# Kernel tuning notes

Hardware: AMD Instinct MI355X
Metric: run time of the kernel (lower is better)

The kernel has to match this reference:

```python
import jax, jax.numpy as jnp
import numpy as np

N, IN, OUT = 8192, 4096, 16384


def setup_inputs() -> dict:
    key = jax.random.key(0)
    kx, kw, kb = jax.random.split(key, 3)
    x = jax.random.normal(kx, (N, IN), dtype=jnp.float32)
    # init matches reset_parameters: normal(0, sqrt(1/in_features))
    weight = jax.random.normal(kw, (OUT, IN), dtype=jnp.float32) * np.sqrt(1.0 / IN)
    bias = jax.random.normal(kb, (OUT,), dtype=jnp.float32) * 0.02
    return {"x": x, "weight": weight, "bias": bias}


def _ternarize(weight):
    # threshold = 0.5 * mean(|W|); zero out |w| < threshold, else sign(w)
    threshold = 0.5 * jnp.mean(jnp.abs(weight))
    keep = jnp.abs(weight) >= threshold
    ternary_weight = jnp.sign(weight) * keep.astype(weight.dtype)
    return ternary_weight


def reference(x, weight, bias):
    tw = _ternarize(weight)              # [out, in] in {-1, 0, 1}
    out = x @ tw.T + bias                # [N, out]
    return out
```

## Files before the change

kernel.cpp:

```cpp
#include <hip/hip_runtime.h>
#include <hip/hip_bf16.h>
#include <cstdint>
#include <cstddef>

#define M_DIM 8192
#define K_DIM 4096
#define N_DIM 16384

#define BM 256
#define BN 256
#define BK 32
#define NT (K_DIM / BK)
#define GX (N_DIM / BN)
#define GY (M_DIM / BM)

typedef __attribute__((ext_vector_type(8))) short short8;
typedef __attribute__((ext_vector_type(4))) float floatx4;

__device__ inline void gl2lds16(const void* g, void* l) {
  __builtin_amdgcn_global_load_lds(
      (const __attribute__((address_space(1))) void*)g,
      (__attribute__((address_space(3))) void*)l, 16, 0, 0);
}

__global__ void abssum_kernel(const float* __restrict__ w, double* __restrict__ out) {
  size_t tid = (size_t)blockIdx.x * blockDim.x + threadIdx.x;
  size_t stride = (size_t)gridDim.x * blockDim.x;
  const float4* w4 = (const float4*)w;
  const size_t n4 = (size_t)N_DIM * K_DIM / 4;
  double s = 0.0;
  for (size_t i = tid; i < n4; i += stride) {
    float4 v = w4[i];
    s += (double)fabsf(v.x) + (double)fabsf(v.y) + (double)fabsf(v.z) + (double)fabsf(v.w);
  }
  #pragma unroll
  for (int off = 32; off > 0; off >>= 1) s += __shfl_down(s, off, 64);
  if ((threadIdx.x & 63) == 0) atomicAdd(out, s);
}

__global__ void ternarize_kernel(const float* __restrict__ w, ushort* __restrict__ tw,
                                 const double* __restrict__ sum) {
  __shared__ float sthr;
  if (threadIdx.x == 0)
    sthr = (float)(0.5 * (*sum) / (double)((size_t)N_DIM * K_DIM));
  __syncthreads();
  const float thr = sthr;
  size_t i = ((size_t)blockIdx.x * blockDim.x + threadIdx.x) * 8;
  float4 a = *(const float4*)(w + i);
  float4 b = *(const float4*)(w + i + 4);
  float v[8] = {a.x, a.y, a.z, a.w, b.x, b.y, b.z, b.w};
  union { ushort u[8]; uint4 q; } o;
  #pragma unroll
  for (int j = 0; j < 8; j++) {
    float av = fabsf(v[j]);
    o.u[j] = (av >= thr) ? ((v[j] > 0.0f) ? (ushort)0x3F80 : (ushort)0xBF80) : (ushort)0;
  }
  *(uint4*)(tw + i) = o.q;
}

__device__ inline ushort f2bf(float f) {
  uint32_t u = __float_as_uint(f);
  return (ushort)((u + 0x7FFFu + ((u >> 16) & 1u)) >> 16);
}
__global__ void bf16cast_kernel(const float* __restrict__ x, ushort* __restrict__ xb) {
  size_t i = ((size_t)blockIdx.x * blockDim.x + threadIdx.x) * 8;
  float4 a = *(const float4*)(x + i);
  float4 b = *(const float4*)(x + i + 4);
  float v[8] = {a.x, a.y, a.z, a.w, b.x, b.y, b.z, b.w};
  union { ushort u[8]; uint4 q; } o;
  #pragma unroll
  for (int j = 0; j < 8; j++) o.u[j] = f2bf(v[j]);
  *(uint4*)(xb + i) = o.q;
}

__global__ __launch_bounds__(512, 2)
void gemm_bt_kernel(const ushort* __restrict__ A, const ushort* __restrict__ B,
                    const float* __restrict__ bias, float* __restrict__ C) {
  __shared__ __align__(128) ushort As[4][BM * BK];
  __shared__ __align__(128) ushort Bs[4][BN * BK];

  const int tid  = threadIdx.x;
  const int wave = tid >> 6;
  const int lane = tid & 63;
  const int wm   = wave >> 2;
  const int wn   = wave & 3;
  const int r16  = lane & 15;
  const int quad = lane >> 4;

  const int f  = (int)(blockIdx.y * GX + blockIdx.x);
  const int xc = f & 7;
  const int j  = f >> 3;
  const int p  = j >> 5;
  const int k  = j & 31;
  const int pm = p >> 2, pn = p & 3;
  const int bm = pm * 16 + ((xc >> 2) << 3) + (k & 7);
  const int bn = pn * 16 + ((xc & 3) << 2) + (k >> 3);

  const int bsw = ((lane >> 2) ^ (lane >> 4)) & 1;
  const int rr  = ((lane >> 3) << 1) | bsw;
  const int qb1 = ((lane >> 1) ^ (lane >> 3)) & 1;
  const int qb0 = (lane ^ (lane >> 2) ^ (lane >> 4)) & 1;
  const int qq  = (qb1 << 1) | qb0;
  const int srow = wave * 16 + rr;
  const int scol = qq * 8;
  const ushort* pA0 = A + (size_t)(bm * BM + srow) * K_DIM + scol;
  const ushort* pA1 = pA0 + (size_t)128 * K_DIM;
  const ushort* pB0 = B + (size_t)(bn * BN + srow) * K_DIM + scol;
  const ushort* pB1 = pB0 + (size_t)128 * K_DIM;
  const int ldsw = wave * 16 * BK;

#define STAGE_A(T) do { const int _b = (T) & 3;                        \
    gl2lds16(pA0 + (size_t)(T) * BK, &As[_b][ldsw]);                   \
    gl2lds16(pA1 + (size_t)(T) * BK, &As[_b][128 * BK + ldsw]); } while (0)
#define STAGE_B(T) do { const int _b = (T) & 3;                        \
    gl2lds16(pB0 + (size_t)(T) * BK, &Bs[_b][ldsw]);                   \
    gl2lds16(pB1 + (size_t)(T) * BK, &Bs[_b][128 * BK + ldsw]); } while (0)

  floatx4 acc[8][4];
  #pragma unroll
  for (int m = 0; m < 8; m++)
    #pragma unroll
    for (int n = 0; n < 4; n++)
      acc[m][n] = (floatx4){0.f, 0.f, 0.f, 0.f};

  STAGE_A(0); STAGE_B(0);
  STAGE_A(1); STAGE_B(1);
  STAGE_A(2); STAGE_B(2);
  STAGE_A(3);
  asm volatile("s_waitcnt vmcnt(10)" ::: "memory");
  __builtin_amdgcn_s_barrier();

  const int inner = ((r16 << 6) + (quad << 4)) ^ ((r16 & 7) << 4);
  const char* aBytes; const char* bBytes;

  for (int t = 0; t < NT; ++t) {
    const int cb = t & 3;
    aBytes = (const char*)(&As[cb][0]) + wm * 8192 + inner;
    bBytes = (const char*)(&Bs[cb][0]) + wn * 4096 + inner;
    short8 a[8], b[4];
    #pragma unroll
    for (int m = 0; m < 4; ++m) a[m] = *(const short8*)(aBytes + m * 1024);
    #pragma unroll
    for (int n = 0; n < 4; ++n) b[n] = *(const short8*)(bBytes + n * 1024);
    __builtin_amdgcn_sched_barrier(0);
    #pragma unroll
    for (int m = 4; m < 8; ++m) a[m] = *(const short8*)(aBytes + m * 1024);
    if (t + 3 < NT) STAGE_B(t + 3);
    __builtin_amdgcn_sched_barrier(0);
    __builtin_amdgcn_s_barrier();
    asm volatile("s_waitcnt lgkmcnt(4)" ::: "memory");
    __builtin_amdgcn_sched_barrier(0);
    __builtin_amdgcn_s_setprio(1);
    #pragma unroll
    for (int m = 0; m < 4; ++m)
      #pragma unroll
      for (int n = 0; n < 4; ++n)
        acc[m][n] = __builtin_amdgcn_mfma_f32_16x16x32_bf16(a[m], b[n], acc[m][n], 0, 0, 0);
    __builtin_amdgcn_s_setprio(0);
    __builtin_amdgcn_s_barrier();
    if (t + 4 < NT) {
      STAGE_A(t + 4);
      asm volatile("s_waitcnt vmcnt(10)" ::: "memory");
    } else {
      asm volatile("s_waitcnt vmcnt(0)" ::: "memory");
    }
    __builtin_amdgcn_s_barrier();
    asm volatile("s_waitcnt lgkmcnt(0)" ::: "memory");
    __builtin_amdgcn_sched_barrier(0);
    __builtin_amdgcn_s_setprio(1);
    #pragma unroll
    for (int m = 4; m < 8; ++m)
      #pragma unroll
      for (int n = 0; n < 4; ++n)
        acc[m][n] = __builtin_amdgcn_mfma_f32_16x16x32_bf16(a[m], b[n], acc[m][n], 0, 0, 0);
    __builtin_amdgcn_s_setprio(0);
    __builtin_amdgcn_s_barrier();
  }

  const int crow = bm * BM + wm * 128 + quad * 4;
  const int ccol = bn * BN + wn * 64 + r16;
  #pragma unroll
  for (int n = 0; n < 4; ++n) {
    const int col = ccol + n * 16;
    const float bv = bias[col];
    #pragma unroll
    for (int m = 0; m < 8; ++m) {
      const size_t row0 = (size_t)(crow + m * 16);
      #pragma unroll
      for (int r = 0; r < 4; ++r)
        __builtin_nontemporal_store(acc[m][n][r] + bv, &C[(row0 + r) * N_DIM + col]);
    }
  }
#undef STAGE_A
#undef STAGE_B
}

extern "C" void kernel_launch(void* const* d_in, const int* in_sizes, int n_in,
                              void* d_out, int out_size, void* d_ws, size_t ws_size,
                              hipStream_t stream) {
  const float* x    = (const float*)d_in[0];
  const float* w    = (const float*)d_in[1];
  const float* bias = (const float*)d_in[2];
  float* out = (float*)d_out;

  char* ws = (char*)d_ws;
  double* sum = (double*)ws;
  ushort* xb  = (ushort*)(ws + 256);
  ushort* tw  = (ushort*)(ws + 256 + (size_t)M_DIM * K_DIM * 2);

  hipMemsetAsync(sum, 0, sizeof(double), stream);
  abssum_kernel<<<2048, 256, 0, stream>>>(w, sum);
  ternarize_kernel<<<(size_t)N_DIM * K_DIM / 8 / 256, 256, 0, stream>>>(w, tw, sum);
  bf16cast_kernel<<<(size_t)M_DIM * K_DIM / 8 / 256, 256, 0, stream>>>(x, xb);

  dim3 grid(GX, GY);
  gemm_bt_kernel<<<grid, 512, 0, stream>>>(xb, tw, bias, out);
}
```

Measured before the change: 1.998 ms.

## Software-pipeline LDS fragment loads across k-tiles and make abs-sum reduction deterministic

The GEMM main loop is restructured so the low-half A fragments and the B fragments for the next k-tile are read from LDS while the current tile's second MFMA half runs. B registers are double-buffered across an unrolled-by-two loop. This hides LDS read latency behind MFMA work but raises register pressure under the 512-thread, 2-block launch bound. Separately, the atomic double accumulation for the weight abs-sum is replaced by per-block partials plus a single-block final reduction, which removes the memset and the atomics.

```diff
diff --git a/kernel.cpp b/kernel.cpp
--- a/kernel.cpp
+++ b/kernel.cpp
@@ -23,7 +23,7 @@
       (__attribute__((address_space(3))) void*)l, 16, 0, 0);
 }
 
-__global__ void abssum_kernel(const float* __restrict__ w, double* __restrict__ out) {
+__global__ void abssum_partial(const float* __restrict__ w, double* __restrict__ part) {
   size_t tid = (size_t)blockIdx.x * blockDim.x + threadIdx.x;
   size_t stride = (size_t)gridDim.x * blockDim.x;
   const float4* w4 = (const float4*)w;
@@ -35,7 +35,23 @@
   }
   #pragma unroll
   for (int off = 32; off > 0; off >>= 1) s += __shfl_down(s, off, 64);
-  if ((threadIdx.x & 63) == 0) atomicAdd(out, s);
+  __shared__ double sred[4];
+  if ((threadIdx.x & 63) == 0) sred[threadIdx.x >> 6] = s;
+  __syncthreads();
+  if (threadIdx.x == 0) part[blockIdx.x] = sred[0] + sred[1] + sred[2] + sred[3];
+}
+
+__global__ void abssum_final(const double* __restrict__ part, double* __restrict__ sum) {
+  const int tid = threadIdx.x;
+  double s = 0.0;
+  #pragma unroll
+  for (int k = 0; k < 8; ++k) s += part[tid + k * 256];
+  #pragma unroll
+  for (int off = 32; off > 0; off >>= 1) s += __shfl_down(s, off, 64);
+  __shared__ double sred[4];
+  if ((tid & 63) == 0) sred[tid >> 6] = s;
+  __syncthreads();
+  if (tid == 0) *sum = sred[0] + sred[1] + sred[2] + sred[3];
 }
 
 __global__ void ternarize_kernel(const float* __restrict__ w, ushort* __restrict__ tw,
@@ -123,58 +139,72 @@
     for (int n = 0; n < 4; n++)
       acc[m][n] = (floatx4){0.f, 0.f, 0.f, 0.f};
 
+  const int inner = ((r16 << 6) + (quad << 4)) ^ ((r16 & 7) << 4);
+#define ABYTES(T) ((const char*)(&As[(T) & 3][0]) + wm * 8192 + inner)
+#define BBYTES(T) ((const char*)(&Bs[(T) & 3][0]) + wn * 4096 + inner)
+
+  short8 al[4], ah[4], bA[4], bB[4];
+
   STAGE_A(0); STAGE_B(0);
   STAGE_A(1); STAGE_B(1);
   STAGE_A(2); STAGE_B(2);
   STAGE_A(3);
   asm volatile("s_waitcnt vmcnt(10)" ::: "memory");
   __builtin_amdgcn_s_barrier();
-
-  const int inner = ((r16 << 6) + (quad << 4)) ^ ((r16 & 7) << 4);
-  const char* aBytes; const char* bBytes;
-
-  for (int t = 0; t < NT; ++t) {
-    const int cb = t & 3;
-    aBytes = (const char*)(&As[cb][0]) + wm * 8192 + inner;
-    bBytes = (const char*)(&Bs[cb][0]) + wn * 4096 + inner;
-    short8 a[8], b[4];
-    #pragma unroll
-    for (int m = 0; m < 4; ++m) a[m] = *(const short8*)(aBytes + m * 1024);
-    #pragma unroll
-    for (int n = 0; n < 4; ++n) b[n] = *(const short8*)(bBytes + n * 1024);
-    __builtin_amdgcn_sched_barrier(0);
-    #pragma unroll
-    for (int m = 4; m < 8; ++m) a[m] = *(const short8*)(aBytes + m * 1024);
-    if (t + 3 < NT) STAGE_B(t + 3);
-    __builtin_amdgcn_sched_barrier(0);
-    __builtin_amdgcn_s_barrier();
-    asm volatile("s_waitcnt lgkmcnt(4)" ::: "memory");
-    __builtin_amdgcn_sched_barrier(0);
-    __builtin_amdgcn_s_setprio(1);
-    #pragma unroll
-    for (int m = 0; m < 4; ++m)
-      #pragma unroll
-      for (int n = 0; n < 4; ++n)
-        acc[m][n] = __builtin_amdgcn_mfma_f32_16x16x32_bf16(a[m], b[n], acc[m][n], 0, 0, 0);
-    __builtin_amdgcn_s_setprio(0);
-    __builtin_amdgcn_s_barrier();
-    if (t + 4 < NT) {
-      STAGE_A(t + 4);
-      asm volatile("s_waitcnt vmcnt(10)" ::: "memory");
-    } else {
-      asm volatile("s_waitcnt vmcnt(0)" ::: "memory");
-    }
-    __builtin_amdgcn_s_barrier();
-    asm volatile("s_waitcnt lgkmcnt(0)" ::: "memory");
-    __builtin_amdgcn_sched_barrier(0);
-    __builtin_amdgcn_s_setprio(1);
-    #pragma unroll
-    for (int m = 4; m < 8; ++m)
-      #pragma unroll
-      for (int n = 0; n < 4; ++n)
-        acc[m][n] = __builtin_amdgcn_mfma_f32_16x16x32_bf16(a[m], b[n], acc[m][n], 0, 0, 0);
-    __builtin_amdgcn_s_setprio(0);
-    __builtin_amdgcn_s_barrier();
+  {
+    const char* aB0 = ABYTES(0);
+    const char* bB0 = BBYTES(0);
+    #pragma unroll
+    for (int m = 0; m < 4; ++m) al[m] = *(const short8*)(aB0 + m * 1024);
+    #pragma unroll
+    for (int n = 0; n < 4; ++n) bA[n] = *(const short8*)(bB0 + n * 1024);
+  }
+
+#define ONE_TILE(T, bcur, bnxt) do {                                               \
+    if ((T) + 3 < NT) STAGE_B((T) + 3);                                            \
+    asm volatile("s_waitcnt lgkmcnt(0)" ::: "memory");   \
+    __builtin_amdgcn_sched_barrier(0);                                             \
+    { const char* _aB = ABYTES(T);                                                 \
+      _Pragma("unroll")                                                            \
+      for (int m = 0; m < 4; ++m)                                                  \
+        ah[m] = *(const short8*)(_aB + (4 + m) * 1024); }                          \
+    __builtin_amdgcn_sched_barrier(0);       \
+    __builtin_amdgcn_s_setprio(1);                                                 \
+    _Pragma("unroll")                                                              \
+    for (int m = 0; m < 4; ++m)                                                    \
+      _Pragma("unroll")                                                            \
+      for (int n = 0; n < 4; ++n)                                                  \
+        acc[m][n] = __builtin_amdgcn_mfma_f32_16x16x32_bf16(al[m], bcur[n], acc[m][n], 0, 0, 0); \
+    __builtin_amdgcn_s_setprio(0);                                                 \
+    asm volatile("s_waitcnt lgkmcnt(0)" ::: "memory");    \
+    __builtin_amdgcn_s_barrier();                                        \
+    if ((T) + 4 < NT) {                                                            \
+      STAGE_A((T) + 4);                                                            \
+      asm volatile("s_waitcnt vmcnt(10)" ::: "memory");      \
+    } else {                                                                       \
+      asm volatile("s_waitcnt vmcnt(0)" ::: "memory");             \
+    }                                                                              \
+    __builtin_amdgcn_s_barrier();                                       \
+    if ((T) + 1 < NT) {                                                            \
+      const char* _aB = ABYTES((T) + 1); const char* _bB = BBYTES((T) + 1);        \
+      _Pragma("unroll")                                                            \
+      for (int m = 0; m < 4; ++m) al[m] = *(const short8*)(_aB + m * 1024);        \
+      _Pragma("unroll")                                                            \
+      for (int n = 0; n < 4; ++n) bnxt[n] = *(const short8*)(_bB + n * 1024);      \
+    }                                                                              \
+    __builtin_amdgcn_sched_barrier(0);      \
+    __builtin_amdgcn_s_setprio(1);                                                 \
+    _Pragma("unroll")                                                              \
+    for (int m = 0; m < 4; ++m)                                                    \
+      _Pragma("unroll")                                                            \
+      for (int n = 0; n < 4; ++n)                                                  \
+        acc[4 + m][n] = __builtin_amdgcn_mfma_f32_16x16x32_bf16(ah[m], bcur[n], acc[4 + m][n], 0, 0, 0); \
+    __builtin_amdgcn_s_setprio(0);                                                 \
+  } while (0)
+
+  for (int t0 = 0; t0 < NT; t0 += 2) {
+    ONE_TILE(t0, bA, bB);
+    ONE_TILE(t0 + 1, bB, bA);
   }
 
   const int crow = bm * BM + wm * 128 + quad * 4;
@@ -191,6 +221,9 @@
         __builtin_nontemporal_store(acc[m][n][r] + bv, &C[(row0 + r) * N_DIM + col]);
     }
   }
+#undef ONE_TILE
+#undef ABYTES
+#undef BBYTES
 #undef STAGE_A
 #undef STAGE_B
 }
@@ -204,12 +237,13 @@
   float* out = (float*)d_out;
 
   char* ws = (char*)d_ws;
-  double* sum = (double*)ws;
-  ushort* xb  = (ushort*)(ws + 256);
-  ushort* tw  = (ushort*)(ws + 256 + (size_t)M_DIM * K_DIM * 2);
-
-  hipMemsetAsync(sum, 0, sizeof(double), stream);
-  abssum_kernel<<<2048, 256, 0, stream>>>(w, sum);
+  double* sum  = (double*)ws;
+  double* part = (double*)(ws + 1024);
+  ushort* xb   = (ushort*)(ws + 32768);
+  ushort* tw   = (ushort*)(ws + 32768 + (size_t)M_DIM * K_DIM * 2);
+
+  abssum_partial<<<2048, 256, 0, stream>>>(w, part);
+  abssum_final<<<1, 256, 0, stream>>>(part, sum);
   ternarize_kernel<<<(size_t)N_DIM * K_DIM / 8 / 256, 256, 0, stream>>>(w, tw, sum);
   bf16cast_kernel<<<(size_t)M_DIM * K_DIM / 8 / 256, 256, 0, stream>>>(x, xb);
 
```

Result: faster. 1.818 ms (-9.0%).
